# Kernel tuning notes

Measured on AMD Instinct MI355X. Metric: run time of the kernel, lower is better.

The kernel has to match this reference:

```python
import jax, jax.numpy as jnp
import numpy as np

N, E, H, C, B = 20000, 320000, 4, 64, 64
D = H * C  # 256, output_dim_gnn
NEG_SLOPE = 0.2
EPS = 1e-5


def setup_inputs() -> dict:
    key = jax.random.key(0)
    ks = iter(jax.random.split(key, 40))
    s = 0.05
    inp = {}
    inp['x'] = jax.random.normal(next(ks), (N, 5), jnp.float32)
    inp['edge_index'] = jax.random.randint(next(ks), (2, E), 0, N, jnp.int64)
    inp['edge_attr'] = jax.random.normal(next(ks), (E, 63), jnp.float32)
    inp['batch'] = jnp.sort(jax.random.randint(next(ks), (N,), 0, B, jnp.int64))
    # node / edge embedding linears
    inp['node_W'] = jax.random.normal(next(ks), (5, D), jnp.float32) * s
    inp['node_b'] = jnp.zeros((D,), jnp.float32)
    inp['edge_W'] = jax.random.normal(next(ks), (63, D), jnp.float32) * s
    inp['edge_b'] = jnp.zeros((D,), jnp.float32)
    # two GATv2 layers + batch norms
    for i in range(2):
        inp[f'Wl{i}'] = jax.random.normal(next(ks), (D, H * C), jnp.float32) * s
        inp[f'bl{i}'] = jnp.zeros((H * C,), jnp.float32)
        inp[f'Wr{i}'] = jax.random.normal(next(ks), (D, H * C), jnp.float32) * s
        inp[f'br{i}'] = jnp.zeros((H * C,), jnp.float32)
        inp[f'We{i}'] = jax.random.normal(next(ks), (D, H * C), jnp.float32) * s
        inp[f'att{i}'] = jax.random.normal(next(ks), (H, C), jnp.float32) * s
        inp[f'bias{i}'] = jnp.zeros((H * C,), jnp.float32)
        inp[f'gamma{i}'] = jnp.ones((D,), jnp.float32)
        inp[f'beta{i}'] = jnp.zeros((D,), jnp.float32)
    # final MLP + output layer
    inp['mlp_W'] = jax.random.normal(next(ks), (D, C), jnp.float32) * s
    inp['mlp_b'] = jnp.zeros((C,), jnp.float32)
    inp['out_W'] = jax.random.normal(next(ks), (C, 5), jnp.float32) * s
    inp['out_b'] = jnp.zeros((5,), jnp.float32)
    return inp


def gatv2_conv(x, src, dst, e, Wl, bl, Wr, br, We, att, bias):
    # x: [N, D]; e: [E, D] (embedded edge features)
    xl = (x @ Wl + bl).reshape(N, H, C)  # source-side transform (lin_l)
    xr = (x @ Wr + br).reshape(N, H, C)  # target-side transform (lin_r)
    ee = (e @ We).reshape(E, H, C)       # lin_edge (no bias in PyG)
    m = xl[src] + xr[dst] + ee           # [E, H, C]
    alpha = jnp.einsum('ehc,hc->eh', jax.nn.leaky_relu(m, NEG_SLOPE), att)
    # segment softmax over incoming edges of each target node
    amax = jax.ops.segment_max(alpha, dst, num_segments=N)[dst]
    ex = jnp.exp(alpha - amax)
    denom = jax.ops.segment_sum(ex, dst, num_segments=N)[dst]
    a = ex / denom                        # [E, H]
    out = jax.ops.segment_sum(xl[src] * a[:, :, None], dst, num_segments=N)
    return out.reshape(N, H * C) + bias


def batch_norm(x, gamma, beta):
    mu = jnp.mean(x, axis=0)
    var = jnp.mean((x - mu) ** 2, axis=0)  # biased var (training-mode norm)
    return (x - mu) * jax.lax.rsqrt(var + EPS) * gamma + beta


def reference(x, edge_index, edge_attr, batch,
              node_W, node_b, edge_W, edge_b,
              Wl0, bl0, Wr0, br0, We0, att0, bias0, gamma0, beta0,
              Wl1, bl1, Wr1, br1, We1, att1, bias1, gamma1, beta1,
              mlp_W, mlp_b, out_W, out_b):
    src, dst = edge_index[0], edge_index[1]
    h = x @ node_W + node_b          # [N, D]
    e = edge_attr @ edge_W + edge_b  # [E, D]
    h = gatv2_conv(h, src, dst, e, Wl0, bl0, Wr0, br0, We0, att0, bias0)
    h = jax.nn.relu(batch_norm(h, gamma0, beta0))
    h = gatv2_conv(h, src, dst, e, Wl1, bl1, Wr1, br1, We1, att1, bias1)
    h = jax.nn.relu(batch_norm(h, gamma1, beta1))
    h = jax.nn.relu(h @ mlp_W + mlp_b)  # [N, C]
    # global mean pool per graph
    pooled = jax.ops.segment_sum(h, batch, num_segments=B)
    cnt = jax.ops.segment_sum(jnp.ones((N,), h.dtype), batch, num_segments=B)
    pooled = pooled / jnp.maximum(cnt, 1.0)[:, None]
    return pooled @ out_W + out_b  # [B, n_classes]
```

## Files before the change

### kernel.cpp

```cpp
#include <hip/hip_runtime.h>

#define NN 20000
#define EE 320000
#define BB 64

typedef _Float16 half8 __attribute__((ext_vector_type(8)));
typedef float floatx4 __attribute__((ext_vector_type(4)));

__global__ void k_prep_edgeW(const float* __restrict__ edge_W, const float* __restrict__ edge_b,
                             const float* __restrict__ We0, const float* __restrict__ We1,
                             _Float16* __restrict__ Wpt0, _Float16* __restrict__ Wpt1) {
    __shared__ float row[256];
    int k = blockIdx.x, layer = blockIdx.y, j = threadIdx.x;
    row[j] = (k < 63) ? edge_W[k*256 + j] : edge_b[j];
    __syncthreads();
    const float* We = layer ? We1 : We0;
    float acc = 0.f;
    for (int t = 0; t < 256; ++t) acc += row[t] * We[t*256 + j];
    (layer ? Wpt1 : Wpt0)[j*64 + k] = (_Float16)acc;
}

__global__ void k_prep_acat(const float* __restrict__ node_W, const float* __restrict__ node_b,
                            const float* __restrict__ Wl0, const float* __restrict__ bl0,
                            const float* __restrict__ Wr0, const float* __restrict__ br0,
                            float* __restrict__ Acat) {
    __shared__ float row[256];
    int k = blockIdx.x, j = threadIdx.x;
    if (j < 256) row[j] = (k < 5) ? node_W[k*256 + j] : node_b[j];
    __syncthreads();
    int jj = j & 255;
    const float* W = (j < 256) ? Wl0 : Wr0;
    float acc = 0.f;
    for (int t = 0; t < 256; ++t) acc += row[t] * W[t*256 + jj];
    if (k == 5) acc += (j < 256) ? bl0[jj] : br0[jj];
    Acat[k*512 + j] = acc;
}

__global__ void k_prep_t16(const float* __restrict__ Wl1, const float* __restrict__ bl1,
                           const float* __restrict__ Wr1, const float* __restrict__ br1,
                           const float* __restrict__ mlp_W,
                           _Float16* __restrict__ WlWr1t, float* __restrict__ blr1,
                           _Float16* __restrict__ mlpWt) {
    int n = blockIdx.x, k = threadIdx.x;
    if (n < 512) {
        float v = (n < 256) ? Wl1[k*256 + n] : Wr1[k*256 + (n - 256)];
        WlWr1t[n*256 + k] = (_Float16)v;
        if (k == 0) blr1[n] = (n < 256) ? bl1[n] : br1[n - 256];
    } else {
        int nn = n - 512;
        mlpWt[nn*256 + k] = (_Float16)mlp_W[k*64 + nn];
    }
}

__global__ void k_hist(const int* __restrict__ ei, int* __restrict__ counts) {
    int e = blockIdx.x*256 + threadIdx.x;
    if (e < EE) atomicAdd(&counts[ei[EE + e]], 1);
}

__global__ __launch_bounds__(1024) void k_scan(const int* __restrict__ counts,
                                               int* __restrict__ row_ptr, int* __restrict__ cursor) {
    __shared__ int part[1024];
    int t = threadIdx.x;
    const int per = (NN + 1023) / 1024;
    int b0 = t*per, b1 = min(b0 + per, NN);
    int s = 0;
    for (int i = b0; i < b1; ++i) s += counts[i];
    part[t] = s; __syncthreads();
    for (int d = 1; d < 1024; d <<= 1) {
        int v = (t >= d) ? part[t-d] : 0;
        __syncthreads();
        part[t] += v;
        __syncthreads();
    }
    int run = (t == 0) ? 0 : part[t-1];
    for (int i = b0; i < b1; ++i) { row_ptr[i] = run; cursor[i] = run; run += counts[i]; }
    if (t == 0) row_ptr[NN] = EE;
}

__global__ void k_scatter(const int* __restrict__ ei, const float* __restrict__ attr,
                          int* __restrict__ cursor, int* __restrict__ csr_src,
                          _Float16* __restrict__ attr16) {
    int tid = threadIdx.x;
    int w = tid >> 6, lane = tid & 63;
    int e = blockIdx.x*4 + w;
    if (e >= EE) return;
    int p;
    if (lane == 0) {
        int d = ei[EE + e];
        p = atomicAdd(&cursor[d], 1);
        csr_src[p] = ei[e];
    }
    p = __shfl(p, 0);
    float v = (lane < 63) ? attr[(size_t)e*63 + lane] : 1.0f;
    attr16[(size_t)p*64 + lane] = (_Float16)v;
}

__global__ void k_xlxr0(const float* __restrict__ x, const float* __restrict__ Acat,
                        _Float16* __restrict__ xlxr16) {
    int n = blockIdx.x, j = threadIdx.x;
    float a0 = Acat[5*512 + j], a1 = Acat[5*512 + 256 + j];
#pragma unroll
    for (int k = 0; k < 5; ++k) {
        float xv = x[n*5 + k];
        a0 += xv * Acat[k*512 + j];
        a1 += xv * Acat[k*512 + 256 + j];
    }
    xlxr16[(size_t)n*512 + j] = (_Float16)a0;
    xlxr16[(size_t)n*512 + 256 + j] = (_Float16)a1;
}

#define NPB 4

#define LOADT(Q) { \
    int er = tl + srow; if (er >= el) er = el - 1; \
    const _Float16* sp = &xlxr16[(size_t)csrc[er]*512 + wave*64 + scol]; \
    rx0[Q] = *(const half8*)&sp[0]; \
    rx1[Q] = *(const half8*)&sp[8]; \
    int arow = tl + l15; if (arow >= el) arow = el - 1; \
    const _Float16* ap = &attr16[(size_t)arow*64]; \
    ra0[Q] = *(const half8*)&ap[l4*8]; \
    ra1[Q] = *(const half8*)&ap[32 + l4*8]; \
    rxr[Q] = (float)xlxr16[(size_t)nl*512 + 256 + wave*64 + lane]; \
}

#define FUSED_BODY(CUR) { \
    int nt = ec - tc; if (nt > 16) nt = 16; \
     \
    floatx4 acc[4]; \
    _Pragma("unroll") \
    for (int ct = 0; ct < 4; ++ct) { \
        floatx4 z = {}; \
        acc[ct] = __builtin_amdgcn_mfma_f32_16x16x32_f16(ra0[CUR], bf[ct][0], z, 0, 0, 0); \
        acc[ct] = __builtin_amdgcn_mfma_f32_16x16x32_f16(ra1[CUR], bf[ct][1], acc[ct], 0, 0, 0); \
    } \
     \
    *(half8*)&xls[wave][srow][scol]     = rx0[CUR]; \
    *(half8*)&xls[wave][srow][scol + 8] = rx1[CUR]; \
     \
    float xrf[4]; \
    _Pragma("unroll") \
    for (int ct = 0; ct < 4; ++ct) xrf[ct] = __shfl(rxr[CUR], ct*16 + l15); \
     \
    if (haveL) { LOADT(CUR); haveL = advL(); } \
     \
    float p[4]; \
    _Pragma("unroll") \
    for (int r = 0; r < 4; ++r) { \
        int eidx = l4*4 + r; \
        float pv = 0.f; \
        _Pragma("unroll") \
        for (int ct = 0; ct < 4; ++ct) { \
            float m = acc[ct][r] + (float)xls[wave][eidx][ct*16 + l15] + xrf[ct]; \
            float lr = (m > 0.f) ? m : 0.2f*m; \
            pv += lr * attv[ct]; \
        } \
        pv += __shfl_xor(pv, 1); \
        pv += __shfl_xor(pv, 2); \
        pv += __shfl_xor(pv, 4); \
        pv += __shfl_xor(pv, 8); \
        p[r] = (eidx < nt) ? pv : -3.0e38f; \
    } \
     \
    float mt = fmaxf(fmaxf(p[0], p[1]), fmaxf(p[2], p[3])); \
    mt = fmaxf(mt, __shfl_xor(mt, 16)); \
    mt = fmaxf(mt, __shfl_xor(mt, 32)); \
    float mnew = fmaxf(m_run, mt); \
    float scale = __expf(m_run - mnew); \
    out_acc *= scale; l_run *= scale; \
     \
    float w4[4]; float wsum = 0.f; \
    _Pragma("unroll") \
    for (int r = 0; r < 4; ++r) { w4[r] = __expf(p[r] - mnew); wsum += w4[r]; } \
    wsum += __shfl_xor(wsum, 16); \
    wsum += __shfl_xor(wsum, 32); \
    l_run += wsum; \
     \
    _Pragma("unroll") \
    for (int k = 0; k < 16; ++k) { \
        float wk = __shfl(w4[k & 3], (k >> 2) << 4); \
        out_acc += wk * (float)xls[wave][k][lane]; \
    } \
    m_run = mnew; \
    if (tc + 16 >= ec) { \
        gat16[(size_t)nc*256 + wave*64 + lane] = (_Float16)(out_acc / l_run); \
        m_run = -3.0e38f; l_run = 0.f; out_acc = 0.f; \
    } \
}

__global__ __launch_bounds__(256) void k_fused(const _Float16* __restrict__ attr16,
        const int* __restrict__ csrc, const int* __restrict__ row_ptr,
        const _Float16* __restrict__ Wpt, const float* __restrict__ att,
        const _Float16* __restrict__ xlxr16, _Float16* __restrict__ gat16) {
    int tid = threadIdx.x;
    int wave = tid >> 6, lane = tid & 63;
    int l15 = lane & 15, l4 = lane >> 4;
    int srow = lane >> 2, scol = (lane & 3) * 16;

    __shared__ __align__(16) _Float16 xls[4][16][72];

    half8 bf[4][2];
    float attv[4];
#pragma unroll
    for (int ct = 0; ct < 4; ++ct) {
        int c = wave*64 + ct*16 + l15;
        attv[ct] = att[c];
        bf[ct][0] = *(const half8*)&Wpt[(size_t)c*64 + l4*8];
        bf[ct][1] = *(const half8*)&Wpt[(size_t)c*64 + 32 + l4*8];
    }

    int n0 = blockIdx.x*NPB;
    int nEnd = n0 + NPB; if (nEnd > NN) nEnd = NN;

    int nc = -1, tc = 0, ec = 0;
    for (int m = n0; m < nEnd; ++m) {
        int s = row_ptr[m], e = row_ptr[m+1];
        if (e <= s) gat16[(size_t)m*256 + wave*64 + lane] = (_Float16)0.f;
        else if (nc < 0) { nc = m; tc = s; ec = e; }
    }
    if (nc < 0) return;

    int nl = nc, tl = tc, el = ec;
    auto advIt = [&](int& n, int& t, int& e) -> bool {
        t += 16;
        if (t < e) return true;
        for (;;) {
            ++n;
            if (n >= nEnd) return false;
            int s = row_ptr[n]; e = row_ptr[n+1];
            if (e > s) { t = s; return true; }
        }
    };
    auto advL = [&]() -> bool { return advIt(nl, tl, el); };

    half8 rx0[2], rx1[2], ra0[2], ra1[2];
    float rxr[2];

    LOADT(0);
    bool haveL = advL();
    if (haveL) { LOADT(1); haveL = advL(); }

    float m_run = -3.0e38f, l_run = 0.f, out_acc = 0.f;
    for (;;) {
        FUSED_BODY(0);
        if (!advIt(nc, tc, ec)) break;
        FUSED_BODY(1);
        if (!advIt(nc, tc, ec)) break;
    }
}

__global__ void k_bn_stats(const _Float16* __restrict__ X, float* __restrict__ stats) {
    int j = threadIdx.x;
    int shard = blockIdx.x & 15;
    float s = 0.f, q = 0.f;
    for (int r = blockIdx.x; r < NN; r += gridDim.x) {
        float v = (float)X[(size_t)r*256 + j];
        s += v; q += v*v;
    }
    atomicAdd(&stats[shard*512 + j], s);
    atomicAdd(&stats[shard*512 + 256 + j], q);
}

__global__ void k_bn_final(const float* __restrict__ stats, const float* __restrict__ gamma,
                           const float* __restrict__ beta, float* __restrict__ ss) {
    int j = threadIdx.x;
    float s = 0.f, q = 0.f;
#pragma unroll
    for (int sh = 0; sh < 16; ++sh) {
        s += stats[sh*512 + j];
        q += stats[sh*512 + 256 + j];
    }
    float mean = s * (1.0f/NN);
    float var  = q * (1.0f/NN) - mean*mean;
    float sc = rsqrtf(var + 1e-5f) * gamma[j];
    ss[j] = sc;
    ss[256 + j] = beta[j] - mean*sc;
}

template<bool RELU, typename OT>
__global__ __launch_bounds__(256) void k_gemm(const _Float16* __restrict__ A,
                       const float* __restrict__ ssv,
                       const _Float16* __restrict__ Bt,
                       const float* __restrict__ bias, OT* __restrict__ C,
                       int M, int ldc) {
    __shared__ __align__(16) _Float16 As[128][72];
    __shared__ __align__(16) _Float16 Bs[64][72];
    int tid = threadIdx.x;
    int wave = tid >> 6, lane = tid & 63;
    int l15 = lane & 15, l4 = lane >> 4;
    int row0 = blockIdx.x*128, n0 = blockIdx.y*64;
    floatx4 acc[2][4] = {};
    for (int k0 = 0; k0 < 256; k0 += 64) {
#pragma unroll
        for (int q = 0; q < 4; ++q) {
            int c = tid + q*256;
            int r = c >> 3, kc = (c & 7)*8;
            int gr = row0 + r; if (gr >= M) gr = M - 1;
            half8 g = *(const half8*)&A[(size_t)gr*256 + k0 + kc];
            _Float16 tmp[8];
#pragma unroll
            for (int i = 0; i < 8; ++i) {
                int colk = k0 + kc + i;
                float v = (float)g[i]*ssv[colk] + ssv[256 + colk];
                tmp[i] = (_Float16)fmaxf(v, 0.f);
            }
            *(half8*)&As[r][kc] = *(half8*)tmp;
        }
#pragma unroll
        for (int q = 0; q < 2; ++q) {
            int c = tid + q*256;
            int r = c >> 3, kc = (c & 7)*8;
            *(half8*)&Bs[r][kc] = *(const half8*)&Bt[(size_t)(n0 + r)*256 + k0 + kc];
        }
        __syncthreads();
#pragma unroll
        for (int ks = 0; ks < 64; ks += 32) {
            half8 a0 = *(const half8*)&As[wave*32 + l15][ks + l4*8];
            half8 a1 = *(const half8*)&As[wave*32 + 16 + l15][ks + l4*8];
#pragma unroll
            for (int nb = 0; nb < 4; ++nb) {
                half8 b = *(const half8*)&Bs[nb*16 + l15][ks + l4*8];
                acc[0][nb] = __builtin_amdgcn_mfma_f32_16x16x32_f16(a0, b, acc[0][nb], 0, 0, 0);
                acc[1][nb] = __builtin_amdgcn_mfma_f32_16x16x32_f16(a1, b, acc[1][nb], 0, 0, 0);
            }
        }
        __syncthreads();
    }
#pragma unroll
    for (int m = 0; m < 2; ++m)
#pragma unroll
    for (int nb = 0; nb < 4; ++nb) {
        int col = n0 + nb*16 + l15;
        float bv = bias[col];
#pragma unroll
        for (int r = 0; r < 4; ++r) {
            int grow = row0 + wave*32 + m*16 + l4*4 + r;
            if (grow < M) {
                float v = acc[m][nb][r] + bv;
                if (RELU) v = fmaxf(v, 0.f);
                C[(size_t)grow*ldc + col] = (OT)v;
            }
        }
    }
}

__global__ void k_pool2(const float* __restrict__ mo, const int* __restrict__ batch,
                        float* __restrict__ pooledDiv) {
    int b = blockIdx.x;
    int j = threadIdx.x & 63, rg = threadIdx.x >> 6;
    int lo = 0, hi = NN;
    while (lo < hi) { int mid = (lo + hi) >> 1; if (batch[mid] < b) lo = mid + 1; else hi = mid; }
    int s = lo;
    lo = 0; hi = NN;
    while (lo < hi) { int mid = (lo + hi) >> 1; if (batch[mid] < b + 1) lo = mid + 1; else hi = mid; }
    int e = lo;
    float acc = 0.f;
    for (int r = s + rg; r < e; r += 4) acc += mo[(size_t)r*64 + j];
    __shared__ float red[256];
    red[threadIdx.x] = acc;
    __syncthreads();
    if (rg == 0) {
        float v = red[j] + red[64 + j] + red[128 + j] + red[192 + j];
        pooledDiv[b*64 + j] = v / fmaxf((float)(e - s), 1.f);
    }
}

__global__ void k_final(const float* __restrict__ pooledDiv,
                        const float* __restrict__ outW, const float* __restrict__ outb,
                        float* __restrict__ out) {
    int t = threadIdx.x;
    if (t >= 320) return;
    int b = t / 5, c = t % 5;
    float acc = outb[c];
    for (int k = 0; k < 64; ++k) acc += pooledDiv[b*64 + k] * outW[k*5 + c];
    out[t] = acc;
}

extern "C" void kernel_launch(void* const* d_in, const int* in_sizes, int n_in,
                              void* d_out, int out_size, void* d_ws, size_t ws_size,
                              hipStream_t stream) {
    const float* x      = (const float*)d_in[0];
    const int*   ei     = (const int*)d_in[1];
    const float* attr   = (const float*)d_in[2];
    const int*   batch  = (const int*)d_in[3];
    const float* node_W = (const float*)d_in[4];
    const float* node_b = (const float*)d_in[5];
    const float* edge_W = (const float*)d_in[6];
    const float* edge_b = (const float*)d_in[7];
    const float* Wl[2]   = {(const float*)d_in[8],  (const float*)d_in[17]};
    const float* bl[2]   = {(const float*)d_in[9],  (const float*)d_in[18]};
    const float* Wr[2]   = {(const float*)d_in[10], (const float*)d_in[19]};
    const float* br[2]   = {(const float*)d_in[11], (const float*)d_in[20]};
    const float* We[2]   = {(const float*)d_in[12], (const float*)d_in[21]};
    const float* att[2]  = {(const float*)d_in[13], (const float*)d_in[22]};
    const float* gamma[2]= {(const float*)d_in[15], (const float*)d_in[24]};
    const float* beta[2] = {(const float*)d_in[16], (const float*)d_in[25]};
    const float* mlp_W = (const float*)d_in[26];
    const float* mlp_b = (const float*)d_in[27];
    const float* out_W = (const float*)d_in[28];
    const float* out_b = (const float*)d_in[29];
    float* out = (float*)d_out;

    char* p = (char*)d_ws;
    size_t off = 0;
    auto carve = [&](size_t bytes) -> void* {
        void* r = p + off;
        off = (off + bytes + 255) & ~(size_t)255;
        return r;
    };
    _Float16* Wpt0   = (_Float16*)carve(256*64*2);
    _Float16* Wpt1   = (_Float16*)carve(256*64*2);
    float*    Acat   = (float*)carve(6*512*4);
    _Float16* WlWr1t = (_Float16*)carve(512*256*2);
    float*    blr1   = (float*)carve(512*4);
    _Float16* mlpWt  = (_Float16*)carve(64*256*2);
    float*    ss     = (float*)carve(512*4);
    _Float16* xlxr16 = (_Float16*)carve((size_t)NN*512*2);
    _Float16* gat16  = (_Float16*)carve((size_t)NN*256*2);
    float*    mlo    = (float*)carve((size_t)NN*64*4);
    _Float16* attr16 = (_Float16*)carve((size_t)EE*64*2);
    int*      row_ptr= (int*)carve((NN+1)*4);
    int*      csrc   = (int*)carve((size_t)EE*4);
    int*      cursor = (int*)carve(NN*4);
    float*    pooledDiv = (float*)carve(BB*64*4);
    char*     zz     = (char*)carve((NN + 16384)*4);
    int*      counts = (int*)zz;
    float*    stats  = (float*)(zz + (size_t)NN*4);
    if (off > ws_size) return;

    hipMemsetAsync(zz, 0, (size_t)(NN + 16384)*4, stream);
    k_prep_edgeW<<<dim3(64,2), 256, 0, stream>>>(edge_W, edge_b, We[0], We[1], Wpt0, Wpt1);
    k_prep_acat<<<6, 512, 0, stream>>>(node_W, node_b, Wl[0], bl[0], Wr[0], br[0], Acat);
    k_prep_t16<<<576, 256, 0, stream>>>(Wl[1], bl[1], Wr[1], br[1], mlp_W, WlWr1t, blr1, mlpWt);
    k_hist<<<(EE+255)/256, 256, 0, stream>>>(ei, counts);
    k_scan<<<1, 1024, 0, stream>>>(counts, row_ptr, cursor);
    k_scatter<<<EE/4, 256, 0, stream>>>(ei, attr, cursor, csrc, attr16);
    k_xlxr0<<<NN, 256, 0, stream>>>(x, Acat, xlxr16);

    for (int L = 0; L < 2; ++L) {
        k_fused<<<(NN + NPB - 1)/NPB, 256, 0, stream>>>(attr16, csrc, row_ptr,
                 L ? Wpt1 : Wpt0, att[L], xlxr16, gat16);
        k_bn_stats<<<1024, 256, 0, stream>>>(gat16, stats + L*8192);
        k_bn_final<<<1, 256, 0, stream>>>(stats + L*8192, gamma[L], beta[L], ss);
        if (L == 0)
            k_gemm<false, _Float16><<<dim3(157, 8), 256, 0, stream>>>(gat16, ss, WlWr1t, blr1, xlxr16, NN, 512);
        else
            k_gemm<true, float><<<dim3(157, 1), 256, 0, stream>>>(gat16, ss, mlpWt, mlp_b, mlo, NN, 64);
    }
    k_pool2<<<BB, 256, 0, stream>>>(mlo, batch, pooledDiv);
    k_final<<<1, 320, 0, stream>>>(pooledDiv, out_W, out_b, out);
}
```

Measured before the change: 472.3 us.

## Fuse BN stats into GAT kernel and cut register pressure for occupancy

```diff
diff --git a/kernel.cpp b/kernel.cpp
--- a/kernel.cpp
+++ b/kernel.cpp
@@ -111,86 +111,23 @@
 
 #define NPB 4
 
-#define LOADT(Q) { \
+#define LOADT() { \
     int er = tl + srow; if (er >= el) er = el - 1; \
     const _Float16* sp = &xlxr16[(size_t)csrc[er]*512 + wave*64 + scol]; \
-    rx0[Q] = *(const half8*)&sp[0]; \
-    rx1[Q] = *(const half8*)&sp[8]; \
+    rx0 = *(const half8*)&sp[0]; \
+    rx1 = *(const half8*)&sp[8]; \
     int arow = tl + l15; if (arow >= el) arow = el - 1; \
     const _Float16* ap = &attr16[(size_t)arow*64]; \
-    ra0[Q] = *(const half8*)&ap[l4*8]; \
-    ra1[Q] = *(const half8*)&ap[32 + l4*8]; \
-    rxr[Q] = (float)xlxr16[(size_t)nl*512 + 256 + wave*64 + lane]; \
-}
-
-#define FUSED_BODY(CUR) { \
-    int nt = ec - tc; if (nt > 16) nt = 16; \
-     \
-    floatx4 acc[4]; \
-    _Pragma("unroll") \
-    for (int ct = 0; ct < 4; ++ct) { \
-        floatx4 z = {}; \
-        acc[ct] = __builtin_amdgcn_mfma_f32_16x16x32_f16(ra0[CUR], bf[ct][0], z, 0, 0, 0); \
-        acc[ct] = __builtin_amdgcn_mfma_f32_16x16x32_f16(ra1[CUR], bf[ct][1], acc[ct], 0, 0, 0); \
-    } \
-     \
-    *(half8*)&xls[wave][srow][scol]     = rx0[CUR]; \
-    *(half8*)&xls[wave][srow][scol + 8] = rx1[CUR]; \
-     \
-    float xrf[4]; \
-    _Pragma("unroll") \
-    for (int ct = 0; ct < 4; ++ct) xrf[ct] = __shfl(rxr[CUR], ct*16 + l15); \
-     \
-    if (haveL) { LOADT(CUR); haveL = advL(); } \
-     \
-    float p[4]; \
-    _Pragma("unroll") \
-    for (int r = 0; r < 4; ++r) { \
-        int eidx = l4*4 + r; \
-        float pv = 0.f; \
-        _Pragma("unroll") \
-        for (int ct = 0; ct < 4; ++ct) { \
-            float m = acc[ct][r] + (float)xls[wave][eidx][ct*16 + l15] + xrf[ct]; \
-            float lr = (m > 0.f) ? m : 0.2f*m; \
-            pv += lr * attv[ct]; \
-        } \
-        pv += __shfl_xor(pv, 1); \
-        pv += __shfl_xor(pv, 2); \
-        pv += __shfl_xor(pv, 4); \
-        pv += __shfl_xor(pv, 8); \
-        p[r] = (eidx < nt) ? pv : -3.0e38f; \
-    } \
-     \
-    float mt = fmaxf(fmaxf(p[0], p[1]), fmaxf(p[2], p[3])); \
-    mt = fmaxf(mt, __shfl_xor(mt, 16)); \
-    mt = fmaxf(mt, __shfl_xor(mt, 32)); \
-    float mnew = fmaxf(m_run, mt); \
-    float scale = __expf(m_run - mnew); \
-    out_acc *= scale; l_run *= scale; \
-     \
-    float w4[4]; float wsum = 0.f; \
-    _Pragma("unroll") \
-    for (int r = 0; r < 4; ++r) { w4[r] = __expf(p[r] - mnew); wsum += w4[r]; } \
-    wsum += __shfl_xor(wsum, 16); \
-    wsum += __shfl_xor(wsum, 32); \
-    l_run += wsum; \
-     \
-    _Pragma("unroll") \
-    for (int k = 0; k < 16; ++k) { \
-        float wk = __shfl(w4[k & 3], (k >> 2) << 4); \
-        out_acc += wk * (float)xls[wave][k][lane]; \
-    } \
-    m_run = mnew; \
-    if (tc + 16 >= ec) { \
-        gat16[(size_t)nc*256 + wave*64 + lane] = (_Float16)(out_acc / l_run); \
-        m_run = -3.0e38f; l_run = 0.f; out_acc = 0.f; \
-    } \
-}
-
-__global__ __launch_bounds__(256) void k_fused(const _Float16* __restrict__ attr16,
+    ra0 = *(const half8*)&ap[l4*8]; \
+    ra1 = *(const half8*)&ap[32 + l4*8]; \
+    rxr = (float)xlxr16[(size_t)nl*512 + 256 + wave*64 + lane]; \
+}
+
+__global__ __launch_bounds__(256, 8) void k_fused(const _Float16* __restrict__ attr16,
         const int* __restrict__ csrc, const int* __restrict__ row_ptr,
         const _Float16* __restrict__ Wpt, const float* __restrict__ att,
-        const _Float16* __restrict__ xlxr16, _Float16* __restrict__ gat16) {
+        const _Float16* __restrict__ xlxr16, _Float16* __restrict__ gat16,
+        float* __restrict__ stats) {
     int tid = threadIdx.x;
     int wave = tid >> 6, lane = tid & 63;
     int l15 = lane & 15, l4 = lane >> 4;
@@ -198,15 +135,10 @@
 
     __shared__ __align__(16) _Float16 xls[4][16][72];
 
-    half8 bf[4][2];
+    const _Float16* bp = Wpt + (size_t)(wave*64 + l15)*64 + l4*8;
     float attv[4];
 #pragma unroll
-    for (int ct = 0; ct < 4; ++ct) {
-        int c = wave*64 + ct*16 + l15;
-        attv[ct] = att[c];
-        bf[ct][0] = *(const half8*)&Wpt[(size_t)c*64 + l4*8];
-        bf[ct][1] = *(const half8*)&Wpt[(size_t)c*64 + 32 + l4*8];
-    }
+    for (int ct = 0; ct < 4; ++ct) attv[ct] = att[wave*64 + ct*16 + l15];
 
     int n0 = blockIdx.x*NPB;
     int nEnd = n0 + NPB; if (nEnd > NN) nEnd = NN;
@@ -230,42 +162,85 @@
             if (e > s) { t = s; return true; }
         }
     };
-    auto advL = [&]() -> bool { return advIt(nl, tl, el); };
-
-    half8 rx0[2], rx1[2], ra0[2], ra1[2];
-    float rxr[2];
-
-    LOADT(0);
-    bool haveL = advL();
-    if (haveL) { LOADT(1); haveL = advL(); }
+
+    half8 rx0, rx1, ra0, ra1;
+    float rxr;
+    LOADT();
+    bool haveL = advIt(nl, tl, el);
 
     float m_run = -3.0e38f, l_run = 0.f, out_acc = 0.f;
+    float sAcc = 0.f, qAcc = 0.f;
     for (;;) {
-        FUSED_BODY(0);
+        int nt = ec - tc; if (nt > 16) nt = 16;
+        *(half8*)&xls[wave][srow][scol]     = rx0;
+        *(half8*)&xls[wave][srow][scol + 8] = rx1;
+        floatx4 acc[4];
+#pragma unroll
+        for (int ct = 0; ct < 4; ++ct) {
+            half8 b0 = *(const half8*)(bp + ct*1024);
+            half8 b1 = *(const half8*)(bp + ct*1024 + 32);
+            floatx4 z = {};
+            acc[ct] = __builtin_amdgcn_mfma_f32_16x16x32_f16(ra0, b0, z, 0, 0, 0);
+            acc[ct] = __builtin_amdgcn_mfma_f32_16x16x32_f16(ra1, b1, acc[ct], 0, 0, 0);
+        }
+        float xrf[4];
+#pragma unroll
+        for (int ct = 0; ct < 4; ++ct) xrf[ct] = __shfl(rxr, ct*16 + l15);
+        if (haveL) { LOADT(); haveL = advIt(nl, tl, el); }
+        float p[4];
+#pragma unroll
+        for (int r = 0; r < 4; ++r) {
+            int eidx = l4*4 + r;
+            float pv = 0.f;
+#pragma unroll
+            for (int ct = 0; ct < 4; ++ct) {
+                float m = acc[ct][r] + (float)xls[wave][eidx][ct*16 + l15] + xrf[ct];
+                float lr = fmaxf(m, 0.2f*m);
+                pv += lr * attv[ct];
+            }
+            pv += __shfl_xor(pv, 1);
+            pv += __shfl_xor(pv, 2);
+            pv += __shfl_xor(pv, 4);
+            pv += __shfl_xor(pv, 8);
+            p[r] = (eidx < nt) ? pv : -3.0e38f;
+        }
+        float mt = fmaxf(fmaxf(p[0], p[1]), fmaxf(p[2], p[3]));
+        mt = fmaxf(mt, __shfl_xor(mt, 16));
+        mt = fmaxf(mt, __shfl_xor(mt, 32));
+        float mnew = fmaxf(m_run, mt);
+        float scale = __expf(m_run - mnew);
+        out_acc *= scale; l_run *= scale;
+        float w4[4]; float wsum = 0.f;
+#pragma unroll
+        for (int r = 0; r < 4; ++r) { w4[r] = __expf(p[r] - mnew); wsum += w4[r]; }
+        wsum += __shfl_xor(wsum, 16);
+        wsum += __shfl_xor(wsum, 32);
+        l_run += wsum;
+#pragma unroll
+        for (int k = 0; k < 16; ++k) {
+            float wk = __shfl(w4[k & 3], (k >> 2) << 4);
+            out_acc += wk * (float)xls[wave][k][lane];
+        }
+        m_run = mnew;
+        if (tc + 16 >= ec) {
+            _Float16 h = (_Float16)(out_acc / l_run);
+            gat16[(size_t)nc*256 + wave*64 + lane] = h;
+            float hv = (float)h;
+            sAcc += hv; qAcc += hv*hv;
+            m_run = -3.0e38f; l_run = 0.f; out_acc = 0.f;
+        }
         if (!advIt(nc, tc, ec)) break;
-        FUSED_BODY(1);
-        if (!advIt(nc, tc, ec)) break;
-    }
-}
-
-__global__ void k_bn_stats(const _Float16* __restrict__ X, float* __restrict__ stats) {
-    int j = threadIdx.x;
-    int shard = blockIdx.x & 15;
-    float s = 0.f, q = 0.f;
-    for (int r = blockIdx.x; r < NN; r += gridDim.x) {
-        float v = (float)X[(size_t)r*256 + j];
-        s += v; q += v*v;
-    }
-    atomicAdd(&stats[shard*512 + j], s);
-    atomicAdd(&stats[shard*512 + 256 + j], q);
+    }
+    int shard = blockIdx.x & 63;
+    atomicAdd(&stats[shard*512 + wave*64 + lane], sAcc);
+    atomicAdd(&stats[shard*512 + 256 + wave*64 + lane], qAcc);
 }
 
 __global__ void k_bn_final(const float* __restrict__ stats, const float* __restrict__ gamma,
                            const float* __restrict__ beta, float* __restrict__ ss) {
     int j = threadIdx.x;
     float s = 0.f, q = 0.f;
-#pragma unroll
-    for (int sh = 0; sh < 16; ++sh) {
+    for (int sh = 0; sh < 64; ++sh) {
         s += stats[sh*512 + j];
         q += stats[sh*512 + 256 + j];
     }
@@ -422,12 +397,12 @@
     int*      csrc   = (int*)carve((size_t)EE*4);
     int*      cursor = (int*)carve(NN*4);
     float*    pooledDiv = (float*)carve(BB*64*4);
-    char*     zz     = (char*)carve((NN + 16384)*4);
+    char*     zz     = (char*)carve((NN + 2*64*512)*4);
     int*      counts = (int*)zz;
     float*    stats  = (float*)(zz + (size_t)NN*4);
     if (off > ws_size) return;
 
-    hipMemsetAsync(zz, 0, (size_t)(NN + 16384)*4, stream);
+    hipMemsetAsync(zz, 0, (size_t)(NN + 2*64*512)*4, stream);
     k_prep_edgeW<<<dim3(64,2), 256, 0, stream>>>(edge_W, edge_b, We[0], We[1], Wpt0, Wpt1);
     k_prep_acat<<<6, 512, 0, stream>>>(node_W, node_b, Wl[0], bl[0], Wr[0], br[0], Acat);
     k_prep_t16<<<576, 256, 0, stream>>>(Wl[1], bl[1], Wr[1], br[1], mlp_W, WlWr1t, blr1, mlpWt);
@@ -438,9 +413,8 @@
 
     for (int L = 0; L < 2; ++L) {
         k_fused<<<(NN + NPB - 1)/NPB, 256, 0, stream>>>(attr16, csrc, row_ptr,
-                 L ? Wpt1 : Wpt0, att[L], xlxr16, gat16);
-        k_bn_stats<<<1024, 256, 0, stream>>>(gat16, stats + L*8192);
-        k_bn_final<<<1, 256, 0, stream>>>(stats + L*8192, gamma[L], beta[L], ss);
+                 L ? Wpt1 : Wpt0, att[L], xlxr16, gat16, stats + L*32768);
+        k_bn_final<<<1, 256, 0, stream>>>(stats + L*32768, gamma[L], beta[L], ss);
         if (L == 0)
             k_gemm<false, _Float16><<<dim3(157, 8), 256, 0, stream>>>(gat16, ss, WlWr1t, blr1, xlxr16, NN, 512);
         else
```

New measurement: 739.7 us. 56.6% more time.
